# Kernel tuning notes

Hardware: AMD Instinct MI355X
Metric: run time of the kernel (lower is better)

The kernel has to match this reference:

```python
import jax, jax.numpy as jnp
import numpy as np

STRIDES = (8, 16, 32, 64)
SIGMA = 8
DG = 4      # deformable groups
K = 3       # kernel size
PAD = 1


def conv2d(x, w, b=None, pad=1):
    out = jax.lax.conv_general_dilated(
        x, w, window_strides=(1, 1), padding=((pad, pad), (pad, pad)),
        dimension_numbers=('NCHW', 'OIHW', 'NCHW'))
    if b is not None:
        out = out + b[None, :, None, None]
    return out


def deform_conv(x, offset, w):
    """DeformConv v1 (no modulation), stride 1, pad 1, 3x3, DG deform groups.
    x: [N,C,H,W], offset: [N, DG*K*K*2, H, W] (per group, per kernel pos: dy,dx),
    w: [O, C, K, K]. Zero padding outside the image for bilinear sampling."""
    N, C, H, W = x.shape
    Cg = C // DG
    O = w.shape[0]
    off = offset.reshape(N, DG, K * K, 2, H, W)
    dy = off[:, :, :, 0]  # [N,DG,9,H,W]
    dx = off[:, :, :, 1]
    kyx = jnp.arange(K, dtype=x.dtype)
    ky = jnp.repeat(kyx, K).reshape(1, 1, K * K, 1, 1)   # row-major kernel order
    kx = jnp.tile(kyx, K).reshape(1, 1, K * K, 1, 1)
    py = jnp.arange(H, dtype=x.dtype).reshape(1, 1, 1, H, 1) - PAD + ky + dy  # [N,DG,9,H,W]
    px = jnp.arange(W, dtype=x.dtype).reshape(1, 1, 1, 1, W) - PAD + kx + dx
    y0 = jnp.floor(py)
    x0 = jnp.floor(px)
    ly = py - y0
    lx = px - x0
    y0i = y0.astype(jnp.int32)
    x0i = x0.astype(jnp.int32)
    xg = x.reshape(N, DG, Cg, H * W)

    def gather(yi, xi):
        valid = ((yi >= 0) & (yi < H) & (xi >= 0) & (xi < W)).astype(x.dtype)
        idx = jnp.clip(yi, 0, H - 1) * W + jnp.clip(xi, 0, W - 1)  # [N,DG,9,H,W]
        idx = jnp.broadcast_to(idx.reshape(N, DG, 1, -1), (N, DG, Cg, K * K * H * W))
        v = jnp.take_along_axis(xg, idx, axis=3).reshape(N, DG, Cg, K * K, H, W)
        return v * valid[:, :, None]  # zero outside image

    w00 = ((1 - ly) * (1 - lx))[:, :, None]
    w01 = ((1 - ly) * lx)[:, :, None]
    w10 = (ly * (1 - lx))[:, :, None]
    w11 = (ly * lx)[:, :, None]
    val = (gather(y0i, x0i) * w00 + gather(y0i, x0i + 1) * w01 +
           gather(y0i + 1, x0i) * w10 + gather(y0i + 1, x0i + 1) * w11)  # [N,DG,Cg,9,H,W]
    wk = w.reshape(O, DG, Cg, K * K)
    return jnp.einsum('ngckhw,ogck->nohw', val, wk)


def setup_inputs() -> dict:
    key = jax.random.key(0)
    ks = jax.random.split(key, 12)
    shapes = [(2, 256, 100, 152), (2, 256, 50, 76), (2, 256, 25, 38), (2, 256, 13, 19)]
    inp = {}
    for i, s in enumerate(shapes):
        inp[f'feat{i}'] = jax.random.normal(ks[i], s, dtype=jnp.float32)
    inp['loc_w'] = jax.random.normal(ks[4], (1, 256, 3, 3), dtype=jnp.float32) * 0.05
    inp['loc_b'] = jnp.zeros((1,), dtype=jnp.float32)
    inp['shape_w'] = jax.random.normal(ks[5], (2, 256, 3, 3), dtype=jnp.float32) * 0.02
    inp['shape_b'] = jnp.zeros((2,), dtype=jnp.float32)
    inp['offset_w'] = jax.random.normal(ks[6], (3 * 3 * 2 * DG, 2, 1, 1), dtype=jnp.float32) * 0.1
    inp['adapt_w'] = jax.random.normal(ks[7], (256, 256, 3, 3), dtype=jnp.float32) * 0.02
    return inp


def reference(feat0, feat1, feat2, feat3, loc_w, loc_b, shape_w, shape_b, offset_w, adapt_w):
    feats = (feat0, feat1, feat2, feat3)
    loc_outs, shape_outs, reformed, adapt_feats = [], [], [], []
    for f, stride in zip(feats, STRIDES):
        loc = jax.nn.sigmoid(conv2d(f, loc_w, loc_b, pad=1))
        sh = conv2d(f, shape_w, shape_b, pad=1)
        # offsets computed from detached shape prediction (1x1 conv, no bias)
        off = conv2d(jax.lax.stop_gradient(sh), offset_w, None, pad=0)
        ad = jax.nn.relu(deform_conv(f, off, adapt_w))
        loc_outs.append(loc)
        shape_outs.append(sh)
        reformed.append(SIGMA * stride * jnp.exp(sh))
        adapt_feats.append(ad)
    return tuple(loc_outs) + tuple(shape_outs) + tuple(reformed) + tuple(adapt_feats)
```

## Files before the change

kernel.cpp:

```cpp
#include <hip/hip_runtime.h>
#include <cmath>

typedef _Float16 h16x2 __attribute__((ext_vector_type(2)));
typedef _Float16 h16x4 __attribute__((ext_vector_type(4)));
typedef _Float16 h16x8 __attribute__((ext_vector_type(8)));
typedef float    f32x4  __attribute__((ext_vector_type(4)));
typedef float    f32x16 __attribute__((ext_vector_type(16)));
typedef unsigned char      u8;
typedef unsigned int       u32;
typedef unsigned long long u64;

#define CK 2304
#define RB 584
#define TP 32

constexpr int  eH[4]   = {100, 50, 25, 13};
constexpr int  eW[4]   = {152, 76, 38, 19};
constexpr long eFTO[4] = {0, 7782400, 9728000, 10214400};
constexpr long eLOC[4] = {0, 30400, 38000, 39900};
constexpr long eSH[4]  = {40394, 101194, 116394, 120194};
constexpr long eREF[4] = {121182, 181982, 197182, 200982};
constexpr long eAD[4]  = {201970, 7984370, 9929970, 10416370};
constexpr float eSS[4] = {64.f, 128.f, 256.f, 512.f};

__device__ __constant__ int cHW[4]  = {15200, 3800, 950, 247};
__device__ __constant__ long cFTO2[4] = {0, 7782400, 9728000, 10214400};

static __device__ __forceinline__ u32 packpair(float w) {
    _Float16 h = (_Float16)w;
    unsigned short u;
    __builtin_memcpy(&u, &h, 2);
    return (u32)u * 0x10001u;
}
static __device__ __forceinline__ h16x2 u2h(u32 v) {
    h16x2 r;
    __builtin_memcpy(&r, &v, 4);
    return r;
}

__global__ void __launch_bounds__(256) wconv_kernel(
    const float* __restrict__ loc_w, const float* __restrict__ shape_w,
    const float* __restrict__ adw,
    u8* __restrict__ wpack, _Float16* __restrict__ lsw)
{
    int i = blockIdx.x * 256 + threadIdx.x;
    if (i < 147456) {
        int b0 = i * 4;
        int u0 = b0 & 7;
        int lane = (b0 >> 3) & 63;
        int t = b0 >> 9;
        int s = t % 36;
        int rest = t / 36;
        int q = rest & 3;
        int mt = rest >> 2;
        int oc = mt * 32 + (lane & 31);
        float w4[4];
        #pragma unroll
        for (int j = 0; j < 4; ++j) {
            int jj = s * 16 + (lane >> 5) * 8 + u0 + j;
            int k = jj >> 6;
            int c = q * 64 + (jj & 63);
            w4[j] = adw[oc * CK + c * 9 + k] * 16.f;
        }
        int r = __builtin_amdgcn_cvt_pk_fp8_f32(w4[0], w4[1], 0, false);
        r = __builtin_amdgcn_cvt_pk_fp8_f32(w4[2], w4[3], r, true);
        ((u32*)wpack)[i] = (u32)r;
    } else if (i < 184320) {
        int i2 = i - 147456;
        int o = i2 / CK;
        int j = i2 - o * CK;
        int k = j >> 8, c = j & 255;
        float v = 0.f;
        if (o == 0)      v = loc_w[c * 9 + k];
        else if (o == 1) v = shape_w[c * 9 + k];
        else if (o == 2) v = shape_w[CK + c * 9 + k];
        lsw[i2] = (_Float16)v;
    }
}

__global__ void __launch_bounds__(256) transpose_kernel(
    const float* __restrict__ f0, const float* __restrict__ f1,
    const float* __restrict__ f2, const float* __restrict__ f3,
    _Float16* __restrict__ ft)
{
    __shared__ float lds[64][65];
    int bid = blockIdx.x, tid = threadIdx.x;
    int lvl = (bid < 1904) ? 0 : (bid < 2384) ? 1 : (bid < 2504) ? 2 : 3;
    int base = (lvl == 0) ? 0 : (lvl == 1) ? 1904 : (lvl == 2) ? 2384 : 2504;
    int nbhw = (lvl == 0) ? 238 : (lvl == 1) ? 60 : (lvl == 2) ? 15 : 4;
    const float* f = (lvl == 0) ? f0 : (lvl == 1) ? f1 : (lvl == 2) ? f2 : f3;
    int HW = cHW[lvl];
    int b = bid - base;
    int bh = b % nbhw;
    int cg = (b / nbhw) & 3;
    int n  = b / (nbhw * 4);
    int hw0 = bh * 64;

    int pxl = tid & 63, cl = tid >> 6;
    int hwr = hw0 + pxl;
    if (hwr < HW) {
        #pragma unroll
        for (int r = 0; r < 16; ++r) {
            int c = r * 4 + cl;
            lds[c][pxl] = f[(long)(n * 256 + cg * 64 + c) * HW + hwr];
        }
    }
    __syncthreads();
    int px2 = tid >> 2, q = tid & 3;
    int hww = hw0 + px2;
    if (hww < HW) {
        _Float16* dst = ft + cFTO2[lvl] + ((long)(n * HW + hww) << 8) + cg * 64 + q * 16;
        #pragma unroll
        for (int j = 0; j < 16; j += 4) {
            h16x4 v;
            v[0] = (_Float16)lds[q * 16 + j + 0][px2];
            v[1] = (_Float16)lds[q * 16 + j + 1][px2];
            v[2] = (_Float16)lds[q * 16 + j + 2][px2];
            v[3] = (_Float16)lds[q * 16 + j + 3][px2];
            *(h16x4*)(dst + j) = v;
        }
    }
}

template<int LVL>
static __device__ __forceinline__ void fused_body(
    int bidl,
    u8 (*buf)[RB], u8 (*wbuf)[4][1024], float* offsm, float (*shm)[2], u32* pxm,
    const _Float16* __restrict__ ft,
    const float* __restrict__ offw,
    const u8* __restrict__ wpack,
    const _Float16* __restrict__ lsw,
    const float* __restrict__ loc_b, const float* __restrict__ shape_b,
    float* __restrict__ out)
{
    constexpr int H = eH[LVL], W = eW[LVL];
    constexpr int HW = H * W;
    constexpr int total = 2 * HW;
    const _Float16* ftl = ft + eFTO[LVL];
    float* loc_o = out + eLOC[LVL];
    float* sh_o  = out + eSH[LVL];
    float* ref_o = out + eREF[LVL];
    float* ad_o  = out + eAD[LVL];

    int tid = threadIdx.x;
    int wv = tid >> 6, lane = tid & 63;
    int nn = lane & 15, c8 = lane >> 4;
    int pix0 = bidl * TP;

    float* redB = (float*)&buf[0][0];

    if (tid < TP) {
        int pix = pix0 + tid;
        u32 m = 0x80000000u;
        if (pix < total) {
            int n = pix / HW;
            int rem = pix - n * HW;
            int hh = rem / W;
            m = (u32)((n << 16) | (hh << 8) | (rem - hh * W));
        }
        pxm[tid] = m;
    }
    if (tid < 144) offsm[tid] = offw[tid];
    __syncthreads();

    {
        int pxt = wv & 1, kq = wv >> 1;
        int p = pxt * 16 + nn;
        u32 pm = pxm[p];
        bool pv = !(pm >> 31);
        int ww = pm & 255, hh = (pm >> 8) & 255, n = (pm >> 16) & 1;
        f32x4 acc = {0.f, 0.f, 0.f, 0.f};
        const _Float16* ar = lsw + nn * CK + kq * 576 + c8 * 8;
        #pragma unroll 6
        for (int s = 0; s < 18; ++s) {
            int j0 = kq * 576 + s * 32;
            int k = j0 >> 8;
            int c = (j0 & 255) + c8 * 8;
            int ky = (k * 171) >> 9;
            int kx = k - ky * 3;
            int y = hh - 1 + ky, x = ww - 1 + kx;
            h16x8 b = {0, 0, 0, 0, 0, 0, 0, 0};
            if (pv && (unsigned)y < (unsigned)H && (unsigned)x < (unsigned)W)
                b = *(const h16x8*)(ftl + ((long)(n * HW + y * W + x) << 8) + c);
            h16x8 a = *(const h16x8*)(ar + s * 32);
            acc = __builtin_amdgcn_mfma_f32_16x16x32_f16(a, b, acc, 0, 0, 0);
        }
        if (c8 == 0) {
            #pragma unroll
            for (int r = 0; r < 3; ++r) redB[(p * 3 + r) * 4 + kq] = acc[r];
        }
    }
    __syncthreads();
    if (tid < 96) {
        int p = tid & 31, r = tid >> 5;
        float s = redB[(p * 3 + r) * 4 + 0] + redB[(p * 3 + r) * 4 + 1]
                + redB[(p * 3 + r) * 4 + 2] + redB[(p * 3 + r) * 4 + 3];
        u32 pm = pxm[p];
        if (!(pm >> 31)) {
            int ww = pm & 255, hh = (pm >> 8) & 255, n = (pm >> 16) & 1;
            long sp = (long)hh * W + ww;
            if (r == 0) {
                s += loc_b[0];
                loc_o[n * HW + sp] = 1.f / (1.f + expf(-s));
            } else {
                s += shape_b[r - 1];
                sh_o[(n * 2 + r - 1) * HW + sp] = s;
                ref_o[(n * 2 + r - 1) * HW + sp] = eSS[LVL] * expf(s);
                shm[p][r - 1] = s;
            }
        }
    }
    __syncthreads();

    int col = lane & 31, khalf = lane >> 5;
    f32x16 acc = {0,0,0,0,0,0,0,0,0,0,0,0,0,0,0,0};

    auto WISSUE = [&](int q, int d) {
        const u8* src = wpack + (((size_t)((wv * 4 + q) * 18 + d)) << 10) + lane * 16;
        __builtin_amdgcn_global_load_lds((const void*)src, (void*)&wbuf[wv][d & 3][0], 16, 0, 0);
    };

    auto STAGE = [&](int q) {
        WISSUE(q, 0); WISSUE(q, 1); WISSUE(q, 2);
        int it8 = lane >> 3, li8 = lane & 7;
        const _Float16* fb = ftl + q * 64 + li8 * 8;
        u32 su_word = 0, su_w00 = 0, su_w01 = 0, su_w10 = 0, su_w11 = 0;
        if (lane < 36) {
            int e = wv * 36 + lane;
            int p = (e * 7282) >> 16;
            int k = e - p * 9;
            u32 pm = pxm[p];
            if (!(pm >> 31)) {
                int ww = pm & 255, hh = (pm >> 8) & 255, n = (pm >> 16) & 1;
                float s0 = shm[p][0], s1 = shm[p][1];
                int gk4 = (q * 9 + k) * 4;
                float dy = offsm[gk4 + 0] * s0 + offsm[gk4 + 1] * s1;
                float dx = offsm[gk4 + 2] * s0 + offsm[gk4 + 3] * s1;
                int ky = (k * 171) >> 9;
                int kx = k - ky * 3;
                float py  = (float)(hh - 1 + ky) + dy;
                float pxf = (float)(ww - 1 + kx) + dx;
                float fy = floorf(py), fx = floorf(pxf);
                float ly = py - fy, lx = pxf - fx;
                int y0 = (int)fy, x0 = (int)fx;
                int y1 = y0 + 1, x1 = x0 + 1;
                float u00 = (1.f - ly) * (1.f - lx);
                float u01 = (1.f - ly) * lx;
                float u10 = ly * (1.f - lx);
                float u11 = ly * lx;
                bool by0 = (unsigned)y0 < (unsigned)H, by1 = (unsigned)y1 < (unsigned)H;
                bool bx0 = (unsigned)x0 < (unsigned)W, bx1 = (unsigned)x1 < (unsigned)W;
                u00 = (by0 && bx0) ? u00 : 0.f;
                u01 = (by0 && bx1) ? u01 : 0.f;
                u10 = (by1 && bx0) ? u10 : 0.f;
                u11 = (by1 && bx1) ? u11 : 0.f;
                int cy0 = min(max(y0, 0), H - 1), cy1 = min(max(y1, 0), H - 1);
                int cx0 = min(max(x0, 0), W - 1), cx1 = min(max(x1, 0), W - 1);
                int i00 = n * HW + cy0 * W + cx0;
                su_word = (u32)i00 | ((u32)(cx1 - cx0) << 30) | ((u32)(cy1 - cy0) << 31);
                su_w00 = packpair(u00); su_w01 = packpair(u01);
                su_w10 = packpair(u10); su_w11 = packpair(u11);
            }
        }
        #pragma unroll
        for (int i = 0; i < 5; ++i) {
            int item = i * 8 + it8;
            if (item >= 36) continue;
            u32 word = __shfl(su_word, item);
            u32 pw00 = __shfl(su_w00, item);
            u32 pw01 = __shfl(su_w01, item);
            u32 pw10 = __shfl(su_w10, item);
            u32 pw11 = __shfl(su_w11, item);
            int e = wv * 36 + item;
            int p = (e * 7282) >> 16;
            int k = e - p * 9;
            int i00 = word & 0x7FFF;
            int b01 = (word >> 30) & 1;
            int i10 = i00 + ((word >> 31) ? W : 0);
            h16x8 v00 = *(const h16x8*)(fb + ((long)i00 << 8));
            h16x8 v01 = *(const h16x8*)(fb + ((long)(i00 + b01) << 8));
            h16x8 v10 = *(const h16x8*)(fb + ((long)i10 << 8));
            h16x8 v11 = *(const h16x8*)(fb + ((long)(i10 + b01) << 8));
            h16x2 w00 = u2h(pw00), w01 = u2h(pw01), w10 = u2h(pw10), w11 = u2h(pw11);
            float cf[8];
            #pragma unroll
            for (int j = 0; j < 4; ++j) {
                h16x2 a00 = {v00[2*j], v00[2*j+1]};
                h16x2 a01 = {v01[2*j], v01[2*j+1]};
                h16x2 a10 = {v10[2*j], v10[2*j+1]};
                h16x2 a11 = {v11[2*j], v11[2*j+1]};
                h16x2 r = a00 * w00 + a01 * w01 + a10 * w10 + a11 * w11;
                cf[2*j]     = (float)r[0];
                cf[2*j + 1] = (float)r[1];
            }
            int lo = __builtin_amdgcn_cvt_pk_fp8_f32(cf[0], cf[1], 0, false);
            lo = __builtin_amdgcn_cvt_pk_fp8_f32(cf[2], cf[3], lo, true);
            int hi = __builtin_amdgcn_cvt_pk_fp8_f32(cf[4], cf[5], 0, false);
            hi = __builtin_amdgcn_cvt_pk_fp8_f32(cf[6], cf[7], hi, true);
            u64 r8 = ((u64)(u32)hi << 32) | (u32)lo;
            *(u64*)&buf[p][k * 64 + li8 * 8] = r8;
        }
    };

    auto GEMM = [&](int q) {
        const u8* bp = &buf[col][khalf * 8];
        #pragma unroll
        for (int d = 0; d < 18; ++d) {
            if (d < 15) {
                WISSUE(q, d + 3);
                asm volatile("s_waitcnt vmcnt(3)" ::: "memory");
            } else if (d == 15) {
                asm volatile("s_waitcnt vmcnt(2)" ::: "memory");
            } else if (d == 16) {
                asm volatile("s_waitcnt vmcnt(1)" ::: "memory");
            } else {
                asm volatile("s_waitcnt vmcnt(0)" ::: "memory");
            }
            const u8* wb = &wbuf[wv][d & 3][0];
            u64 w0 = *(const u64*)(wb + (lane << 3));
            u64 w1 = *(const u64*)(wb + 512 + (lane << 3));
            u64 b0 = *(const u64*)(bp + (2 * d) * 16);
            u64 b1 = *(const u64*)(bp + (2 * d + 1) * 16);
            acc = __builtin_amdgcn_mfma_f32_32x32x16_fp8_fp8((long)w0, (long)b0, acc, 0, 0, 0);
            acc = __builtin_amdgcn_mfma_f32_32x32x16_fp8_fp8((long)w1, (long)b1, acc, 0, 0, 0);
        }
    };

    STAGE(0);
    __syncthreads();
    GEMM(0);
    __syncthreads();
    STAGE(1);
    __syncthreads();
    GEMM(1);
    __syncthreads();
    STAGE(2);
    __syncthreads();
    GEMM(2);
    __syncthreads();
    STAGE(3);
    __syncthreads();
    GEMM(3);

    {
        u32 pm = pxm[col];
        if (!(pm >> 31)) {
            int ww = pm & 255, hh = (pm >> 8) & 255, n = (pm >> 16) & 1;
            float* ob = ad_o + ((long)(n * 256 + wv * 32)) * HW + (long)hh * W + ww;
            #pragma unroll
            for (int reg = 0; reg < 16; ++reg) {
                int row = (reg & 3) + 8 * (reg >> 2) + 4 * khalf;
                float v = acc[reg] * 0.0625f;
                ob[(long)row * HW] = v > 0.f ? v : 0.f;
            }
        }
    }
}

__global__ void __launch_bounds__(512, 4) fused_kernel(
    const _Float16* __restrict__ ft,
    const float* __restrict__ offw,
    const u8* __restrict__ wpack,
    const _Float16* __restrict__ lsw,
    const float* __restrict__ loc_b, const float* __restrict__ shape_b,
    float* __restrict__ out)
{
    __shared__ u8 buf[TP][RB];
    __shared__ u8 wbuf[8][4][1024];
    __shared__ float offsm[144];
    __shared__ float shm[TP][2];
    __shared__ u32 pxm[TP];

    int bid0 = blockIdx.x;
    int bid = (bid0 & 7) * 158 + (bid0 >> 3);
    if (bid < 950)
        fused_body<0>(bid,         buf, wbuf, offsm, shm, pxm, ft, offw, wpack, lsw, loc_b, shape_b, out);
    else if (bid < 1188)
        fused_body<1>(bid - 950,   buf, wbuf, offsm, shm, pxm, ft, offw, wpack, lsw, loc_b, shape_b, out);
    else if (bid < 1248)
        fused_body<2>(bid - 1188,  buf, wbuf, offsm, shm, pxm, ft, offw, wpack, lsw, loc_b, shape_b, out);
    else
        fused_body<3>(bid - 1248,  buf, wbuf, offsm, shm, pxm, ft, offw, wpack, lsw, loc_b, shape_b, out);
}

extern "C" void kernel_launch(void* const* d_in, const int* in_sizes, int n_in,
                              void* d_out, int out_size, void* d_ws, size_t ws_size,
                              hipStream_t stream)
{
    const float* f0 = (const float*)d_in[0];
    const float* f1 = (const float*)d_in[1];
    const float* f2 = (const float*)d_in[2];
    const float* f3 = (const float*)d_in[3];
    const float* loc_w    = (const float*)d_in[4];
    const float* loc_b    = (const float*)d_in[5];
    const float* shape_w  = (const float*)d_in[6];
    const float* shape_b  = (const float*)d_in[7];
    const float* offset_w = (const float*)d_in[8];
    const float* adapt_w  = (const float*)d_in[9];
    float* out = (float*)d_out;

    u8* wpack      = (u8*)d_ws;
    _Float16* lsw  = (_Float16*)((char*)d_ws + 589824);
    _Float16* ft   = (_Float16*)((char*)d_ws + 663552);

    wconv_kernel<<<720, 256, 0, stream>>>(loc_w, shape_w, adapt_w, wpack, lsw);
    transpose_kernel<<<2536, 256, 0, stream>>>(f0, f1, f2, f3, ft);
    fused_kernel<<<1264, 512, 0, stream>>>(ft, offset_w, wpack, lsw, loc_b, shape_b, out);
}
```

Baseline: 120.4 us.

## Double pixel tile to 64 per block and reuse weight fragments across two accumulators

Raises the pixel tile from 32 to 64 per block, so each wave's fp8 weight fragment loaded via LDS now feeds two MFMA accumulators (two 32-pixel column groups). The loc/shape conv is repartitioned over 4 pixel groups by 2 K-halves, bilinear staging runs twice per wave, and the grid is halved. The aim is to halve weight streaming from global memory per output pixel. In exchange it doubles LDS for the staging buffer, raises register pressure (two f32x16 accumulators) and leaves fewer blocks, which may reduce occupancy and tail balance.

Measured after the change: 139.9 us. +16.2%, slower.

```diff
diff --git a/kernel.cpp b/kernel.cpp
--- a/kernel.cpp
+++ b/kernel.cpp
@@ -12,7 +12,7 @@
 
 #define CK 2304
 #define RB 584
-#define TP 32
+#define TP 64
 
 constexpr int  eH[4]   = {100, 50, 25, 13};
 constexpr int  eW[4]   = {152, 76, 38, 19};
@@ -164,16 +164,16 @@
     __syncthreads();
 
     {
-        int pxt = wv & 1, kq = wv >> 1;
+        int pxt = wv & 3, kq = wv >> 2;
         int p = pxt * 16 + nn;
         u32 pm = pxm[p];
         bool pv = !(pm >> 31);
         int ww = pm & 255, hh = (pm >> 8) & 255, n = (pm >> 16) & 1;
         f32x4 acc = {0.f, 0.f, 0.f, 0.f};
-        const _Float16* ar = lsw + nn * CK + kq * 576 + c8 * 8;
+        const _Float16* ar = lsw + nn * CK + kq * 1152 + c8 * 8;
         #pragma unroll 6
-        for (int s = 0; s < 18; ++s) {
-            int j0 = kq * 576 + s * 32;
+        for (int s = 0; s < 36; ++s) {
+            int j0 = kq * 1152 + s * 32;
             int k = j0 >> 8;
             int c = (j0 & 255) + c8 * 8;
             int ky = (k * 171) >> 9;
@@ -187,14 +187,13 @@
         }
         if (c8 == 0) {
             #pragma unroll
-            for (int r = 0; r < 3; ++r) redB[(p * 3 + r) * 4 + kq] = acc[r];
-        }
-    }
-    __syncthreads();
-    if (tid < 96) {
-        int p = tid & 31, r = tid >> 5;
-        float s = redB[(p * 3 + r) * 4 + 0] + redB[(p * 3 + r) * 4 + 1]
-                + redB[(p * 3 + r) * 4 + 2] + redB[(p * 3 + r) * 4 + 3];
+            for (int r = 0; r < 3; ++r) redB[(p * 3 + r) * 2 + kq] = acc[r];
+        }
+    }
+    __syncthreads();
+    if (tid < 192) {
+        int p = tid & 63, r = tid >> 6;
+        float s = redB[(p * 3 + r) * 2 + 0] + redB[(p * 3 + r) * 2 + 1];
         u32 pm = pxm[p];
         if (!(pm >> 31)) {
             int ww = pm & 255, hh = (pm >> 8) & 255, n = (pm >> 16) & 1;
@@ -213,7 +212,8 @@
     __syncthreads();
 
     int col = lane & 31, khalf = lane >> 5;
-    f32x16 acc = {0,0,0,0,0,0,0,0,0,0,0,0,0,0,0,0};
+    f32x16 acc0 = {0,0,0,0,0,0,0,0,0,0,0,0,0,0,0,0};
+    f32x16 acc1 = {0,0,0,0,0,0,0,0,0,0,0,0,0,0,0,0};
 
     auto WISSUE = [&](int q, int d) {
         const u8* src = wpack + (((size_t)((wv * 4 + q) * 18 + d)) << 10) + lane * 16;
@@ -224,86 +224,90 @@
         WISSUE(q, 0); WISSUE(q, 1); WISSUE(q, 2);
         int it8 = lane >> 3, li8 = lane & 7;
         const _Float16* fb = ftl + q * 64 + li8 * 8;
-        u32 su_word = 0, su_w00 = 0, su_w01 = 0, su_w10 = 0, su_w11 = 0;
-        if (lane < 36) {
-            int e = wv * 36 + lane;
-            int p = (e * 7282) >> 16;
-            int k = e - p * 9;
-            u32 pm = pxm[p];
-            if (!(pm >> 31)) {
-                int ww = pm & 255, hh = (pm >> 8) & 255, n = (pm >> 16) & 1;
-                float s0 = shm[p][0], s1 = shm[p][1];
-                int gk4 = (q * 9 + k) * 4;
-                float dy = offsm[gk4 + 0] * s0 + offsm[gk4 + 1] * s1;
-                float dx = offsm[gk4 + 2] * s0 + offsm[gk4 + 3] * s1;
-                int ky = (k * 171) >> 9;
-                int kx = k - ky * 3;
-                float py  = (float)(hh - 1 + ky) + dy;
-                float pxf = (float)(ww - 1 + kx) + dx;
-                float fy = floorf(py), fx = floorf(pxf);
-                float ly = py - fy, lx = pxf - fx;
-                int y0 = (int)fy, x0 = (int)fx;
-                int y1 = y0 + 1, x1 = x0 + 1;
-                float u00 = (1.f - ly) * (1.f - lx);
-                float u01 = (1.f - ly) * lx;
-                float u10 = ly * (1.f - lx);
-                float u11 = ly * lx;
-                bool by0 = (unsigned)y0 < (unsigned)H, by1 = (unsigned)y1 < (unsigned)H;
-                bool bx0 = (unsigned)x0 < (unsigned)W, bx1 = (unsigned)x1 < (unsigned)W;
-                u00 = (by0 && bx0) ? u00 : 0.f;
-                u01 = (by0 && bx1) ? u01 : 0.f;
-                u10 = (by1 && bx0) ? u10 : 0.f;
-                u11 = (by1 && bx1) ? u11 : 0.f;
-                int cy0 = min(max(y0, 0), H - 1), cy1 = min(max(y1, 0), H - 1);
-                int cx0 = min(max(x0, 0), W - 1), cx1 = min(max(x1, 0), W - 1);
-                int i00 = n * HW + cy0 * W + cx0;
-                su_word = (u32)i00 | ((u32)(cx1 - cx0) << 30) | ((u32)(cy1 - cy0) << 31);
-                su_w00 = packpair(u00); su_w01 = packpair(u01);
-                su_w10 = packpair(u10); su_w11 = packpair(u11);
-            }
-        }
         #pragma unroll
-        for (int i = 0; i < 5; ++i) {
-            int item = i * 8 + it8;
-            if (item >= 36) continue;
-            u32 word = __shfl(su_word, item);
-            u32 pw00 = __shfl(su_w00, item);
-            u32 pw01 = __shfl(su_w01, item);
-            u32 pw10 = __shfl(su_w10, item);
-            u32 pw11 = __shfl(su_w11, item);
-            int e = wv * 36 + item;
-            int p = (e * 7282) >> 16;
-            int k = e - p * 9;
-            int i00 = word & 0x7FFF;
-            int b01 = (word >> 30) & 1;
-            int i10 = i00 + ((word >> 31) ? W : 0);
-            h16x8 v00 = *(const h16x8*)(fb + ((long)i00 << 8));
-            h16x8 v01 = *(const h16x8*)(fb + ((long)(i00 + b01) << 8));
-            h16x8 v10 = *(const h16x8*)(fb + ((long)i10 << 8));
-            h16x8 v11 = *(const h16x8*)(fb + ((long)(i10 + b01) << 8));
-            h16x2 w00 = u2h(pw00), w01 = u2h(pw01), w10 = u2h(pw10), w11 = u2h(pw11);
-            float cf[8];
+        for (int rep = 0; rep < 2; ++rep) {
+            u32 su_word = 0, su_w00 = 0, su_w01 = 0, su_w10 = 0, su_w11 = 0;
+            if (lane < 36) {
+                int e = wv * 72 + rep * 36 + lane;
+                int p = (e * 7282) >> 16;
+                int k = e - p * 9;
+                u32 pm = pxm[p];
+                if (!(pm >> 31)) {
+                    int ww = pm & 255, hh = (pm >> 8) & 255, n = (pm >> 16) & 1;
+                    float s0 = shm[p][0], s1 = shm[p][1];
+                    int gk4 = (q * 9 + k) * 4;
+                    float dy = offsm[gk4 + 0] * s0 + offsm[gk4 + 1] * s1;
+                    float dx = offsm[gk4 + 2] * s0 + offsm[gk4 + 3] * s1;
+                    int ky = (k * 171) >> 9;
+                    int kx = k - ky * 3;
+                    float py  = (float)(hh - 1 + ky) + dy;
+                    float pxf = (float)(ww - 1 + kx) + dx;
+                    float fy = floorf(py), fx = floorf(pxf);
+                    float ly = py - fy, lx = pxf - fx;
+                    int y0 = (int)fy, x0 = (int)fx;
+                    int y1 = y0 + 1, x1 = x0 + 1;
+                    float u00 = (1.f - ly) * (1.f - lx);
+                    float u01 = (1.f - ly) * lx;
+                    float u10 = ly * (1.f - lx);
+                    float u11 = ly * lx;
+                    bool by0 = (unsigned)y0 < (unsigned)H, by1 = (unsigned)y1 < (unsigned)H;
+                    bool bx0 = (unsigned)x0 < (unsigned)W, bx1 = (unsigned)x1 < (unsigned)W;
+                    u00 = (by0 && bx0) ? u00 : 0.f;
+                    u01 = (by0 && bx1) ? u01 : 0.f;
+                    u10 = (by1 && bx0) ? u10 : 0.f;
+                    u11 = (by1 && bx1) ? u11 : 0.f;
+                    int cy0 = min(max(y0, 0), H - 1), cy1 = min(max(y1, 0), H - 1);
+                    int cx0 = min(max(x0, 0), W - 1), cx1 = min(max(x1, 0), W - 1);
+                    int i00 = n * HW + cy0 * W + cx0;
+                    su_word = (u32)i00 | ((u32)(cx1 - cx0) << 30) | ((u32)(cy1 - cy0) << 31);
+                    su_w00 = packpair(u00); su_w01 = packpair(u01);
+                    su_w10 = packpair(u10); su_w11 = packpair(u11);
+                }
+            }
             #pragma unroll
-            for (int j = 0; j < 4; ++j) {
-                h16x2 a00 = {v00[2*j], v00[2*j+1]};
-                h16x2 a01 = {v01[2*j], v01[2*j+1]};
-                h16x2 a10 = {v10[2*j], v10[2*j+1]};
-                h16x2 a11 = {v11[2*j], v11[2*j+1]};
-                h16x2 r = a00 * w00 + a01 * w01 + a10 * w10 + a11 * w11;
-                cf[2*j]     = (float)r[0];
-                cf[2*j + 1] = (float)r[1];
-            }
-            int lo = __builtin_amdgcn_cvt_pk_fp8_f32(cf[0], cf[1], 0, false);
-            lo = __builtin_amdgcn_cvt_pk_fp8_f32(cf[2], cf[3], lo, true);
-            int hi = __builtin_amdgcn_cvt_pk_fp8_f32(cf[4], cf[5], 0, false);
-            hi = __builtin_amdgcn_cvt_pk_fp8_f32(cf[6], cf[7], hi, true);
-            u64 r8 = ((u64)(u32)hi << 32) | (u32)lo;
-            *(u64*)&buf[p][k * 64 + li8 * 8] = r8;
+            for (int i = 0; i < 5; ++i) {
+                int item = i * 8 + it8;
+                if (item >= 36) continue;
+                u32 word = __shfl(su_word, item);
+                u32 pw00 = __shfl(su_w00, item);
+                u32 pw01 = __shfl(su_w01, item);
+                u32 pw10 = __shfl(su_w10, item);
+                u32 pw11 = __shfl(su_w11, item);
+                int e = wv * 72 + rep * 36 + item;
+                int p = (e * 7282) >> 16;
+                int k = e - p * 9;
+                int i00 = word & 0x7FFF;
+                int b01 = (word >> 30) & 1;
+                int i10 = i00 + ((word >> 31) ? W : 0);
+                h16x8 v00 = *(const h16x8*)(fb + ((long)i00 << 8));
+                h16x8 v01 = *(const h16x8*)(fb + ((long)(i00 + b01) << 8));
+                h16x8 v10 = *(const h16x8*)(fb + ((long)i10 << 8));
+                h16x8 v11 = *(const h16x8*)(fb + ((long)(i10 + b01) << 8));
+                h16x2 w00 = u2h(pw00), w01 = u2h(pw01), w10 = u2h(pw10), w11 = u2h(pw11);
+                float cf[8];
+                #pragma unroll
+                for (int j = 0; j < 4; ++j) {
+                    h16x2 a00 = {v00[2*j], v00[2*j+1]};
+                    h16x2 a01 = {v01[2*j], v01[2*j+1]};
+                    h16x2 a10 = {v10[2*j], v10[2*j+1]};
+                    h16x2 a11 = {v11[2*j], v11[2*j+1]};
+                    h16x2 r = a00 * w00 + a01 * w01 + a10 * w10 + a11 * w11;
+                    cf[2*j]     = (float)r[0];
+                    cf[2*j + 1] = (float)r[1];
+                }
+                int lo = __builtin_amdgcn_cvt_pk_fp8_f32(cf[0], cf[1], 0, false);
+                lo = __builtin_amdgcn_cvt_pk_fp8_f32(cf[2], cf[3], lo, true);
+                int hi = __builtin_amdgcn_cvt_pk_fp8_f32(cf[4], cf[5], 0, false);
+                hi = __builtin_amdgcn_cvt_pk_fp8_f32(cf[6], cf[7], hi, true);
+                u64 r8 = ((u64)(u32)hi << 32) | (u32)lo;
+                *(u64*)&buf[p][k * 64 + li8 * 8] = r8;
+            }
         }
     };
 
     auto GEMM = [&](int q) {
-        const u8* bp = &buf[col][khalf * 8];
+        const u8* bp0 = &buf[col][khalf * 8];
+        const u8* bp1 = &buf[32 + col][khalf * 8];
         #pragma unroll
         for (int d = 0; d < 18; ++d) {
             if (d < 15) {
@@ -319,10 +323,14 @@
             const u8* wb = &wbuf[wv][d & 3][0];
             u64 w0 = *(const u64*)(wb + (lane << 3));
             u64 w1 = *(const u64*)(wb + 512 + (lane << 3));
-            u64 b0 = *(const u64*)(bp + (2 * d) * 16);
-            u64 b1 = *(const u64*)(bp + (2 * d + 1) * 16);
-            acc = __builtin_amdgcn_mfma_f32_32x32x16_fp8_fp8((long)w0, (long)b0, acc, 0, 0, 0);
-            acc = __builtin_amdgcn_mfma_f32_32x32x16_fp8_fp8((long)w1, (long)b1, acc, 0, 0, 0);
+            u64 b00 = *(const u64*)(bp0 + (2 * d) * 16);
+            u64 b01 = *(const u64*)(bp0 + (2 * d + 1) * 16);
+            u64 b10 = *(const u64*)(bp1 + (2 * d) * 16);
+            u64 b11 = *(const u64*)(bp1 + (2 * d + 1) * 16);
+            acc0 = __builtin_amdgcn_mfma_f32_32x32x16_fp8_fp8((long)w0, (long)b00, acc0, 0, 0, 0);
+            acc1 = __builtin_amdgcn_mfma_f32_32x32x16_fp8_fp8((long)w0, (long)b10, acc1, 0, 0, 0);
+            acc0 = __builtin_amdgcn_mfma_f32_32x32x16_fp8_fp8((long)w1, (long)b01, acc0, 0, 0, 0);
+            acc1 = __builtin_amdgcn_mfma_f32_32x32x16_fp8_fp8((long)w1, (long)b11, acc1, 0, 0, 0);
         }
     };
 
@@ -350,7 +358,18 @@
             #pragma unroll
             for (int reg = 0; reg < 16; ++reg) {
                 int row = (reg & 3) + 8 * (reg >> 2) + 4 * khalf;
-                float v = acc[reg] * 0.0625f;
+                float v = acc0[reg] * 0.0625f;
+                ob[(long)row * HW] = v > 0.f ? v : 0.f;
+            }
+        }
+        pm = pxm[32 + col];
+        if (!(pm >> 31)) {
+            int ww = pm & 255, hh = (pm >> 8) & 255, n = (pm >> 16) & 1;
+            float* ob = ad_o + ((long)(n * 256 + wv * 32)) * HW + (long)hh * W + ww;
+            #pragma unroll
+            for (int reg = 0; reg < 16; ++reg) {
+                int row = (reg & 3) + 8 * (reg >> 2) + 4 * khalf;
+                float v = acc1[reg] * 0.0625f;
                 ob[(long)row * HW] = v > 0.f ? v : 0.f;
             }
         }
@@ -372,15 +391,15 @@
     __shared__ u32 pxm[TP];
 
     int bid0 = blockIdx.x;
-    int bid = (bid0 & 7) * 158 + (bid0 >> 3);
-    if (bid < 950)
-        fused_body<0>(bid,         buf, wbuf, offsm, shm, pxm, ft, offw, wpack, lsw, loc_b, shape_b, out);
-    else if (bid < 1188)
-        fused_body<1>(bid - 950,   buf, wbuf, offsm, shm, pxm, ft, offw, wpack, lsw, loc_b, shape_b, out);
-    else if (bid < 1248)
-        fused_body<2>(bid - 1188,  buf, wbuf, offsm, shm, pxm, ft, offw, wpack, lsw, loc_b, shape_b, out);
+    int bid = (bid0 & 7) * 79 + (bid0 >> 3);
+    if (bid < 475)
+        fused_body<0>(bid,        buf, wbuf, offsm, shm, pxm, ft, offw, wpack, lsw, loc_b, shape_b, out);
+    else if (bid < 594)
+        fused_body<1>(bid - 475,  buf, wbuf, offsm, shm, pxm, ft, offw, wpack, lsw, loc_b, shape_b, out);
+    else if (bid < 624)
+        fused_body<2>(bid - 594,  buf, wbuf, offsm, shm, pxm, ft, offw, wpack, lsw, loc_b, shape_b, out);
     else
-        fused_body<3>(bid - 1248,  buf, wbuf, offsm, shm, pxm, ft, offw, wpack, lsw, loc_b, shape_b, out);
+        fused_body<3>(bid - 624,  buf, wbuf, offsm, shm, pxm, ft, offw, wpack, lsw, loc_b, shape_b, out);
 }
 
 extern "C" void kernel_launch(void* const* d_in, const int* in_sizes, int n_in,
@@ -405,5 +424,5 @@
 
     wconv_kernel<<<720, 256, 0, stream>>>(loc_w, shape_w, adapt_w, wpack, lsw);
     transpose_kernel<<<2536, 256, 0, stream>>>(f0, f1, f2, f3, ft);
-    fused_kernel<<<1264, 512, 0, stream>>>(ft, offset_w, wpack, lsw, loc_b, shape_b, out);
-}
+    fused_kernel<<<632, 512, 0, stream>>>(ft, offset_w, wpack, lsw, loc_b, shape_b, out);
+}
```

## Double-buffer deformable sampling staging and overlap it with fp8 MFMA GEMM

Applied to the files above, without the earlier changes.

The deformable-group sampling buffer is now double-buffered, so the bilinear gathers for group q+1 are issued and combined in between the MFMA steps of group q's GEMM, with hand-tuned vmcnt waits. This removes the serialized STAGE/GEMM phases and three of the block barriers. The loc/shape 3x3 conv loop also software-prefetches its next B operand. In exchange the shared buffer doubles in size (about 37KB to 55KB+ LDS) and register pressure rises, which may reduce occupancy under launch_bounds(512,4). The vmcnt counting is also fragile.

After: 123.3 us. 2.4% more time.

```diff
diff --git a/kernel.cpp b/kernel.cpp
--- a/kernel.cpp
+++ b/kernel.cpp
@@ -125,7 +125,7 @@
 template<int LVL>
 static __device__ __forceinline__ void fused_body(
     int bidl,
-    u8 (*buf)[RB], u8 (*wbuf)[4][1024], float* offsm, float (*shm)[2], u32* pxm,
+    u8 (*buf)[TP][RB], u8 (*wbuf)[4][1024], float* offsm, float (*shm)[2], u32* pxm,
     const _Float16* __restrict__ ft,
     const float* __restrict__ offw,
     const u8* __restrict__ wpack,
@@ -146,8 +146,9 @@
     int wv = tid >> 6, lane = tid & 63;
     int nn = lane & 15, c8 = lane >> 4;
     int pix0 = bidl * TP;
-
-    float* redB = (float*)&buf[0][0];
+    int it8 = lane >> 3, li8 = lane & 7;
+
+    float* redB = (float*)&buf[0][0][0];
 
     if (tid < TP) {
         int pix = pix0 + tid;
@@ -171,8 +172,7 @@
         int ww = pm & 255, hh = (pm >> 8) & 255, n = (pm >> 16) & 1;
         f32x4 acc = {0.f, 0.f, 0.f, 0.f};
         const _Float16* ar = lsw + nn * CK + kq * 576 + c8 * 8;
-        #pragma unroll 6
-        for (int s = 0; s < 18; ++s) {
+        auto bload = [&](int s) -> h16x8 {
             int j0 = kq * 576 + s * 32;
             int k = j0 >> 8;
             int c = (j0 & 255) + c8 * 8;
@@ -182,8 +182,15 @@
             h16x8 b = {0, 0, 0, 0, 0, 0, 0, 0};
             if (pv && (unsigned)y < (unsigned)H && (unsigned)x < (unsigned)W)
                 b = *(const h16x8*)(ftl + ((long)(n * HW + y * W + x) << 8) + c);
+            return b;
+        };
+        h16x8 bcur = bload(0);
+        #pragma unroll
+        for (int s = 0; s < 18; ++s) {
+            h16x8 bnx = (s < 17) ? bload(s + 1) : (h16x8){0,0,0,0,0,0,0,0};
             h16x8 a = *(const h16x8*)(ar + s * 32);
-            acc = __builtin_amdgcn_mfma_f32_16x16x32_f16(a, b, acc, 0, 0, 0);
+            acc = __builtin_amdgcn_mfma_f32_16x16x32_f16(a, bcur, acc, 0, 0, 0);
+            bcur = bnx;
         }
         if (c8 == 0) {
             #pragma unroll
@@ -220,11 +227,9 @@
         __builtin_amdgcn_global_load_lds((const void*)src, (void*)&wbuf[wv][d & 3][0], 16, 0, 0);
     };
 
-    auto STAGE = [&](int q) {
-        WISSUE(q, 0); WISSUE(q, 1); WISSUE(q, 2);
-        int it8 = lane >> 3, li8 = lane & 7;
-        const _Float16* fb = ftl + q * 64 + li8 * 8;
-        u32 su_word = 0, su_w00 = 0, su_w01 = 0, su_w10 = 0, su_w11 = 0;
+    auto SETUP = [&](int qq, u32& su_word, u32& su_w00, u32& su_w01,
+                     u32& su_w10, u32& su_w11) {
+        su_word = 0; su_w00 = 0; su_w01 = 0; su_w10 = 0; su_w11 = 0;
         if (lane < 36) {
             int e = wv * 36 + lane;
             int p = (e * 7282) >> 16;
@@ -233,7 +238,7 @@
             if (!(pm >> 31)) {
                 int ww = pm & 255, hh = (pm >> 8) & 255, n = (pm >> 16) & 1;
                 float s0 = shm[p][0], s1 = shm[p][1];
-                int gk4 = (q * 9 + k) * 4;
+                int gk4 = (qq * 9 + k) * 4;
                 float dy = offsm[gk4 + 0] * s0 + offsm[gk4 + 1] * s1;
                 float dx = offsm[gk4 + 2] * s0 + offsm[gk4 + 3] * s1;
                 int ky = (k * 171) >> 9;
@@ -262,25 +267,31 @@
                 su_w10 = packpair(u10); su_w11 = packpair(u11);
             }
         }
+    };
+
+    {
+        u32 sw, s00, s01, s10, s11;
+        SETUP(0, sw, s00, s01, s10, s11);
+        const _Float16* fb = ftl + 0 * 64 + li8 * 8;
         #pragma unroll
         for (int i = 0; i < 5; ++i) {
             int item = i * 8 + it8;
             if (item >= 36) continue;
-            u32 word = __shfl(su_word, item);
-            u32 pw00 = __shfl(su_w00, item);
-            u32 pw01 = __shfl(su_w01, item);
-            u32 pw10 = __shfl(su_w10, item);
-            u32 pw11 = __shfl(su_w11, item);
+            u32 word = __shfl(sw, item);
+            u32 pw00 = __shfl(s00, item);
+            u32 pw01 = __shfl(s01, item);
+            u32 pw10 = __shfl(s10, item);
+            u32 pw11 = __shfl(s11, item);
             int e = wv * 36 + item;
             int p = (e * 7282) >> 16;
             int k = e - p * 9;
             int i00 = word & 0x7FFF;
-            int b01 = (word >> 30) & 1;
+            int bb = (word >> 30) & 1;
             int i10 = i00 + ((word >> 31) ? W : 0);
             h16x8 v00 = *(const h16x8*)(fb + ((long)i00 << 8));
-            h16x8 v01 = *(const h16x8*)(fb + ((long)(i00 + b01) << 8));
+            h16x8 v01 = *(const h16x8*)(fb + ((long)(i00 + bb) << 8));
             h16x8 v10 = *(const h16x8*)(fb + ((long)i10 << 8));
-            h16x8 v11 = *(const h16x8*)(fb + ((long)(i10 + b01) << 8));
+            h16x8 v11 = *(const h16x8*)(fb + ((long)(i10 + bb) << 8));
             h16x2 w00 = u2h(pw00), w01 = u2h(pw01), w10 = u2h(pw10), w11 = u2h(pw11);
             float cf[8];
             #pragma unroll
@@ -298,23 +309,97 @@
             int hi = __builtin_amdgcn_cvt_pk_fp8_f32(cf[4], cf[5], 0, false);
             hi = __builtin_amdgcn_cvt_pk_fp8_f32(cf[6], cf[7], hi, true);
             u64 r8 = ((u64)(u32)hi << 32) | (u32)lo;
-            *(u64*)&buf[p][k * 64 + li8 * 8] = r8;
-        }
-    };
-
-    auto GEMM = [&](int q) {
-        const u8* bp = &buf[col][khalf * 8];
+            *(u64*)&buf[0][p][k * 64 + li8 * 8] = r8;
+        }
+    }
+    __syncthreads();
+
+    #pragma unroll
+    for (int q = 0; q < 4; ++q) {
+        const int cur = q & 1, nxt = (q + 1) & 1;
+        WISSUE(q, 0); WISSUE(q, 1); WISSUE(q, 2);
+
+        u32 sw = 0, s00 = 0, s01 = 0, s10 = 0, s11 = 0;
+        if (q < 3) SETUP(q + 1, sw, s00, s01, s10, s11);
+        const _Float16* fb = ftl + (q + 1) * 64 + li8 * 8;
+
+        h16x8 rA00, rA01, rA10, rA11;
+        h16x8 rB00, rB01, rB10, rB11;
+        bool aA = false, aB = false;
+
+        auto QLOAD = [&](int r, h16x8& v00, h16x8& v01, h16x8& v10, h16x8& v11,
+                         bool& act) {
+            int item = r * 8 + it8;
+            act = item < 36;
+            u32 word = __shfl(sw, act ? item : 35);
+            int i00 = word & 0x7FFF;
+            int bb = (word >> 30) & 1;
+            int i10 = i00 + ((word >> 31) ? W : 0);
+            if (act) {
+                v00 = *(const h16x8*)(fb + ((long)i00 << 8));
+                v01 = *(const h16x8*)(fb + ((long)(i00 + bb) << 8));
+                v10 = *(const h16x8*)(fb + ((long)i10 << 8));
+                v11 = *(const h16x8*)(fb + ((long)(i10 + bb) << 8));
+            }
+        };
+        auto QCOMB = [&](int r, h16x8& v00, h16x8& v01, h16x8& v10, h16x8& v11,
+                         bool act) {
+            int item = r * 8 + it8;
+            u32 pw00 = __shfl(s00, act ? item : 35);
+            u32 pw01 = __shfl(s01, act ? item : 35);
+            u32 pw10 = __shfl(s10, act ? item : 35);
+            u32 pw11 = __shfl(s11, act ? item : 35);
+            if (!act) return;
+            h16x2 w00 = u2h(pw00), w01 = u2h(pw01), w10 = u2h(pw10), w11 = u2h(pw11);
+            float cf[8];
+            #pragma unroll
+            for (int j = 0; j < 4; ++j) {
+                h16x2 a00 = {v00[2*j], v00[2*j+1]};
+                h16x2 a01 = {v01[2*j], v01[2*j+1]};
+                h16x2 a10 = {v10[2*j], v10[2*j+1]};
+                h16x2 a11 = {v11[2*j], v11[2*j+1]};
+                h16x2 r2 = a00 * w00 + a01 * w01 + a10 * w10 + a11 * w11;
+                cf[2*j]     = (float)r2[0];
+                cf[2*j + 1] = (float)r2[1];
+            }
+            int lo = __builtin_amdgcn_cvt_pk_fp8_f32(cf[0], cf[1], 0, false);
+            lo = __builtin_amdgcn_cvt_pk_fp8_f32(cf[2], cf[3], lo, true);
+            int hi = __builtin_amdgcn_cvt_pk_fp8_f32(cf[4], cf[5], 0, false);
+            hi = __builtin_amdgcn_cvt_pk_fp8_f32(cf[6], cf[7], hi, true);
+            u64 r8 = ((u64)(u32)hi << 32) | (u32)lo;
+            int e = wv * 36 + item;
+            int p = (e * 7282) >> 16;
+            int k = e - p * 9;
+            *(u64*)&buf[nxt][p][k * 64 + li8 * 8] = r8;
+        };
+
+        const u8* bp = &buf[cur][col][khalf * 8];
         #pragma unroll
         for (int d = 0; d < 18; ++d) {
-            if (d < 15) {
-                WISSUE(q, d + 3);
-                asm volatile("s_waitcnt vmcnt(3)" ::: "memory");
-            } else if (d == 15) {
-                asm volatile("s_waitcnt vmcnt(2)" ::: "memory");
-            } else if (d == 16) {
-                asm volatile("s_waitcnt vmcnt(1)" ::: "memory");
+            if (d < 15) WISSUE(q, d + 3);
+            if (q < 3) {
+                if (d == 3 || d == 5 || d == 7 || d == 9)
+                    asm volatile("s_waitcnt vmcnt(11)" ::: "memory");
+                else if (d == 1 || d == 2 || d == 4 || d == 6 || d == 8 ||
+                         d == 10 || d == 11)
+                    asm volatile("s_waitcnt vmcnt(7)" ::: "memory");
+                else if (d <= 14)
+                    asm volatile("s_waitcnt vmcnt(3)" ::: "memory");
+                else if (d == 15)
+                    asm volatile("s_waitcnt vmcnt(2)" ::: "memory");
+                else if (d == 16)
+                    asm volatile("s_waitcnt vmcnt(1)" ::: "memory");
+                else
+                    asm volatile("s_waitcnt vmcnt(0)" ::: "memory");
             } else {
-                asm volatile("s_waitcnt vmcnt(0)" ::: "memory");
+                if (d <= 14)
+                    asm volatile("s_waitcnt vmcnt(3)" ::: "memory");
+                else if (d == 15)
+                    asm volatile("s_waitcnt vmcnt(2)" ::: "memory");
+                else if (d == 16)
+                    asm volatile("s_waitcnt vmcnt(1)" ::: "memory");
+                else
+                    asm volatile("s_waitcnt vmcnt(0)" ::: "memory");
             }
             const u8* wb = &wbuf[wv][d & 3][0];
             u64 w0 = *(const u64*)(wb + (lane << 3));
@@ -323,24 +408,21 @@
             u64 b1 = *(const u64*)(bp + (2 * d + 1) * 16);
             acc = __builtin_amdgcn_mfma_f32_32x32x16_fp8_fp8((long)w0, (long)b0, acc, 0, 0, 0);
             acc = __builtin_amdgcn_mfma_f32_32x32x16_fp8_fp8((long)w1, (long)b1, acc, 0, 0, 0);
-        }
-    };
-
-    STAGE(0);
-    __syncthreads();
-    GEMM(0);
-    __syncthreads();
-    STAGE(1);
-    __syncthreads();
-    GEMM(1);
-    __syncthreads();
-    STAGE(2);
-    __syncthreads();
-    GEMM(2);
-    __syncthreads();
-    STAGE(3);
-    __syncthreads();
-    GEMM(3);
+            if (q < 3) {
+                if (d == 4)  QCOMB(0, rA00, rA01, rA10, rA11, aA);
+                if (d == 6)  QCOMB(1, rB00, rB01, rB10, rB11, aB);
+                if (d == 8)  QCOMB(2, rA00, rA01, rA10, rA11, aA);
+                if (d == 10) QCOMB(3, rB00, rB01, rB10, rB11, aB);
+                if (d == 12) QCOMB(4, rA00, rA01, rA10, rA11, aA);
+                if (d == 0)  QLOAD(0, rA00, rA01, rA10, rA11, aA);
+                if (d == 2)  QLOAD(1, rB00, rB01, rB10, rB11, aB);
+                if (d == 4)  QLOAD(2, rA00, rA01, rA10, rA11, aA);
+                if (d == 6)  QLOAD(3, rB00, rB01, rB10, rB11, aB);
+                if (d == 8)  QLOAD(4, rA00, rA01, rA10, rA11, aA);
+            }
+        }
+        __syncthreads();
+    }
 
     {
         u32 pm = pxm[col];
@@ -365,7 +447,7 @@
     const float* __restrict__ loc_b, const float* __restrict__ shape_b,
     float* __restrict__ out)
 {
-    __shared__ u8 buf[TP][RB];
+    __shared__ u8 buf[2][TP][RB];
     __shared__ u8 wbuf[8][4][1024];
     __shared__ float offsm[144];
     __shared__ float shm[TP][2];
```

## Stage bilinear corner gathers through LDS with async global_load_lds pipeline

Applied to the files above, without the earlier changes.

Changes the deformable sampling stage so the four bilinear corner vectors are fetched with asynchronous global_load_lds into the per-wave weight ring buffer, with loads for later items in flight while earlier ones are interpolated. This targets the latency of the direct global gathers that were previously issued and consumed together. The weight prefetch for the GEMM is moved to after the gather pipeline. In exchange, only half the lanes do the interpolation math, and the weight prefetch now starts later, so the first GEMM steps may stall more.

New measurement: 159.3 us. 32.3% more time.

```diff
diff --git a/kernel.cpp b/kernel.cpp
--- a/kernel.cpp
+++ b/kernel.cpp
@@ -221,9 +221,6 @@
     };
 
     auto STAGE = [&](int q) {
-        WISSUE(q, 0); WISSUE(q, 1); WISSUE(q, 2);
-        int it8 = lane >> 3, li8 = lane & 7;
-        const _Float16* fb = ftl + q * 64 + li8 * 8;
         u32 su_word = 0, su_w00 = 0, su_w01 = 0, su_w10 = 0, su_w11 = 0;
         if (lane < 36) {
             int e = wv * 36 + lane;
@@ -262,44 +259,69 @@
                 su_w10 = packpair(u10); su_w11 = packpair(u11);
             }
         }
+
+        const _Float16* ftq = ftl + q * 64;
+        int ds2  = lane >> 5;
+        int dcor = (lane >> 3) & 3;
+        int dk8  = lane & 7;
+        auto GISSUE = [&](int g) {
+            int item = 2 * g + ds2;
+            u32 word = __shfl(su_word, item);
+            int i00 = word & 0x7FFF;
+            int b01 = (word >> 30) & 1;
+            int idx = i00 + ((dcor & 2) ? ((word >> 31) ? W : 0) : 0)
+                          + ((dcor & 1) ? b01 : 0);
+            const _Float16* src = ftq + ((long)idx << 8) + dk8 * 8;
+            __builtin_amdgcn_global_load_lds((const void*)src,
+                (void*)&wbuf[wv][g & 3][0], 16, 0, 0);
+        };
+        GISSUE(0); GISSUE(1); GISSUE(2); GISSUE(3);
+
+        int cs  = lane >> 4;
+        int cs2 = (lane >> 3) & 1;
+        int ck8 = lane & 7;
         #pragma unroll
-        for (int i = 0; i < 5; ++i) {
-            int item = i * 8 + it8;
-            if (item >= 36) continue;
-            u32 word = __shfl(su_word, item);
+        for (int j = 0; j < 9; ++j) {
+            if (j < 8) asm volatile("s_waitcnt vmcnt(2)" ::: "memory");
+            else       asm volatile("s_waitcnt vmcnt(0)" ::: "memory");
+            int item = 4 * j + cs * 2 + cs2;
             u32 pw00 = __shfl(su_w00, item);
             u32 pw01 = __shfl(su_w01, item);
             u32 pw10 = __shfl(su_w10, item);
             u32 pw11 = __shfl(su_w11, item);
-            int e = wv * 36 + item;
-            int p = (e * 7282) >> 16;
-            int k = e - p * 9;
-            int i00 = word & 0x7FFF;
-            int b01 = (word >> 30) & 1;
-            int i10 = i00 + ((word >> 31) ? W : 0);
-            h16x8 v00 = *(const h16x8*)(fb + ((long)i00 << 8));
-            h16x8 v01 = *(const h16x8*)(fb + ((long)(i00 + b01) << 8));
-            h16x8 v10 = *(const h16x8*)(fb + ((long)i10 << 8));
-            h16x8 v11 = *(const h16x8*)(fb + ((long)(i10 + b01) << 8));
-            h16x2 w00 = u2h(pw00), w01 = u2h(pw01), w10 = u2h(pw10), w11 = u2h(pw11);
-            float cf[8];
-            #pragma unroll
-            for (int j = 0; j < 4; ++j) {
-                h16x2 a00 = {v00[2*j], v00[2*j+1]};
-                h16x2 a01 = {v01[2*j], v01[2*j+1]};
-                h16x2 a10 = {v10[2*j], v10[2*j+1]};
-                h16x2 a11 = {v11[2*j], v11[2*j+1]};
-                h16x2 r = a00 * w00 + a01 * w01 + a10 * w10 + a11 * w11;
-                cf[2*j]     = (float)r[0];
-                cf[2*j + 1] = (float)r[1];
+            if (lane < 32) {
+                int g = 2 * j + cs;
+                const u8* sb = &wbuf[wv][g & 3][0];
+                h16x8 v00 = *(const h16x8*)(sb + (cs2 * 32 + 0  + ck8) * 16);
+                h16x8 v01 = *(const h16x8*)(sb + (cs2 * 32 + 8  + ck8) * 16);
+                h16x8 v10 = *(const h16x8*)(sb + (cs2 * 32 + 16 + ck8) * 16);
+                h16x8 v11 = *(const h16x8*)(sb + (cs2 * 32 + 24 + ck8) * 16);
+                h16x2 w00 = u2h(pw00), w01 = u2h(pw01), w10 = u2h(pw10), w11 = u2h(pw11);
+                float cf[8];
+                #pragma unroll
+                for (int jj = 0; jj < 4; ++jj) {
+                    h16x2 a00 = {v00[2*jj], v00[2*jj+1]};
+                    h16x2 a01 = {v01[2*jj], v01[2*jj+1]};
+                    h16x2 a10 = {v10[2*jj], v10[2*jj+1]};
+                    h16x2 a11 = {v11[2*jj], v11[2*jj+1]};
+                    h16x2 r = a00 * w00 + a01 * w01 + a10 * w10 + a11 * w11;
+                    cf[2*jj]     = (float)r[0];
+                    cf[2*jj + 1] = (float)r[1];
+                }
+                int lo = __builtin_amdgcn_cvt_pk_fp8_f32(cf[0], cf[1], 0, false);
+                lo = __builtin_amdgcn_cvt_pk_fp8_f32(cf[2], cf[3], lo, true);
+                int hi = __builtin_amdgcn_cvt_pk_fp8_f32(cf[4], cf[5], 0, false);
+                hi = __builtin_amdgcn_cvt_pk_fp8_f32(cf[6], cf[7], hi, true);
+                u64 r8 = ((u64)(u32)hi << 32) | (u32)lo;
+                int e = wv * 36 + item;
+                int p = (e * 7282) >> 16;
+                int k = e - p * 9;
+                *(u64*)&buf[p][k * 64 + ck8 * 8] = r8;
             }
-            int lo = __builtin_amdgcn_cvt_pk_fp8_f32(cf[0], cf[1], 0, false);
-            lo = __builtin_amdgcn_cvt_pk_fp8_f32(cf[2], cf[3], lo, true);
-            int hi = __builtin_amdgcn_cvt_pk_fp8_f32(cf[4], cf[5], 0, false);
-            hi = __builtin_amdgcn_cvt_pk_fp8_f32(cf[6], cf[7], hi, true);
-            u64 r8 = ((u64)(u32)hi << 32) | (u32)lo;
-            *(u64*)&buf[p][k * 64 + li8 * 8] = r8;
-        }
+            __builtin_amdgcn_sched_barrier(0);
+            if (j < 7) { GISSUE(2 * j + 4); GISSUE(2 * j + 5); }
+        }
+        WISSUE(q, 0); WISSUE(q, 1); WISSUE(q, 2);
     };
 
     auto GEMM = [&](int q) {
```
